# Performance work log

Hardware: AMD Instinct MI355X
Metric: run time of the kernel (lower is better)

The kernel has to match this reference:

```python
import jax, jax.numpy as jnp
import numpy as np

NEG_SLOPE = 0.2

def _gatv2_layer(x, src, tgt, Wl, Wr, att, bias, num_nodes, heads, ch):
    # x: [N, Fin]; src/tgt: [E] (self loops already included)
    xl = (x @ Wl).reshape(num_nodes, heads, ch)  # source transform [N,H,C]
    xr = (x @ Wr).reshape(num_nodes, heads, ch)  # target transform [N,H,C]
    m = xl[src] + xr[tgt]                        # [E,H,C]
    m = jnp.where(m > 0, m, NEG_SLOPE * m)       # LeakyReLU
    e = jnp.einsum('ehc,hc->eh', m, att)         # attention logits [E,H]
    # softmax over incoming edges of each target node (numerically stable)
    e_max = jax.ops.segment_max(e, tgt, num_segments=num_nodes)
    e_max = jnp.where(jnp.isfinite(e_max), e_max, 0.0)
    alpha = jnp.exp(e - e_max[tgt])              # [E,H]
    denom = jax.ops.segment_sum(alpha, tgt, num_segments=num_nodes)
    alpha = alpha / (denom[tgt] + 1e-16)
    out = jax.ops.segment_sum(alpha[:, :, None] * xl[src], tgt, num_segments=num_nodes)  # [N,H,C]
    return out.mean(axis=1) + bias               # concat=False -> mean over heads, then bias


def setup_inputs() -> dict:
    key = jax.random.key(0)
    ks = jax.random.split(key, 12)
    N, E = 50000, 800000
    IN, HID, H = 128, 64, 2
    features = jax.random.normal(ks[0], (N, IN), dtype=jnp.float32)
    edge_index = jax.random.randint(ks[1], (2, E), 0, N, dtype=jnp.int64)
    s = 0.1
    return {
        'features': features,
        'edge_index': edge_index,
        'Wl1': jax.random.normal(ks[2], (IN, H * HID), dtype=jnp.float32) * s,
        'Wr1': jax.random.normal(ks[3], (IN, H * HID), dtype=jnp.float32) * s,
        'att1': jax.random.normal(ks[4], (H, HID), dtype=jnp.float32) * s,
        'b1': jnp.zeros((HID,), dtype=jnp.float32),
        'Wl2': jax.random.normal(ks[5], (HID, H * HID), dtype=jnp.float32) * s,
        'Wr2': jax.random.normal(ks[6], (HID, H * HID), dtype=jnp.float32) * s,
        'att2': jax.random.normal(ks[7], (H, HID), dtype=jnp.float32) * s,
        'b2': jnp.zeros((HID,), dtype=jnp.float32),
    }


def reference(features, edge_index, Wl1, Wr1, att1, b1, Wl2, Wr2, att2, b2):
    N = features.shape[0]
    H, HID = att1.shape
    # PyG GATv2Conv default add_self_loops=True
    loop = jnp.arange(N, dtype=edge_index.dtype)
    src = jnp.concatenate([edge_index[0], loop])
    tgt = jnp.concatenate([edge_index[1], loop])
    h = _gatv2_layer(features, src, tgt, Wl1, Wr1, att1, b1, N, H, HID)
    h = jax.nn.relu(h)
    out = _gatv2_layer(h, src, tgt, Wl2, Wr2, att2, b2, N, H, HID)
    return out  # node_mask in original is None
```

## Files before the change

kernel.cpp:

```cpp
#include <hip/hip_runtime.h>
#include <hip/hip_bf16.h>
#include <math.h>


#define HEADS 2
#define CH 64
#define FDIM (HEADS * CH)
#define CAP 48
#define HBLK 3328

typedef _Float16 f16_t;
typedef _Float16 f16x4 __attribute__((ext_vector_type(4)));
typedef _Float16 f16x8 __attribute__((ext_vector_type(8)));
typedef float f32x4 __attribute__((ext_vector_type(4)));
typedef float f32x2 __attribute__((ext_vector_type(2)));


__global__ __launch_bounds__(256)
void init_kernel(const float* __restrict__ Wl1, const float* __restrict__ Wr1,
                 const float* __restrict__ Wl2, const float* __restrict__ Wr2,
                 f16_t* __restrict__ fl1, f16_t* __restrict__ fr1,
                 f16_t* __restrict__ fl2, f16_t* __restrict__ fr2,
                 int* __restrict__ cnt, int N) {
    int bx = blockIdx.x;
    if (bx < 4) {
        const float* W; f16_t* F; int K;
        switch (bx) {
            case 0:  W = Wl1; F = fl1; K = 128; break;
            case 1:  W = Wr1; F = fr1; K = 128; break;
            case 2:  W = Wl2; F = fl2; K = 64;  break;
            default: W = Wr2; F = fr2; K = 64;  break;
        }
        int S = K >> 5;
        int total = 8 * S * 64;
        for (int idx = threadIdx.x; idx < total; idx += blockDim.x) {
            int l  = idx & 63;
            int ts = idx >> 6;
            int s  = ts % S;
            int t  = ts / S;
            int n  = t * 16 + (l & 15);
            int k0 = s * 32 + (l >> 4) * 8;
            f16x8 v;
            #pragma unroll
            for (int j = 0; j < 8; ++j) v[j] = (f16_t)W[(size_t)(k0 + j) * 128 + n];
            *(f16x8*)(F + (size_t)idx * 8) = v;
        }
    } else {
        int n4 = (N + 3) >> 2;
        int stride = (gridDim.x - 4) * blockDim.x;
        for (int i = (bx - 4) * blockDim.x + threadIdx.x; i < n4; i += stride) {
            int i0 = i * 4;
            if (i0 + 3 < N) *(int4*)(cnt + i0) = make_int4(0, 0, 0, 0);
            else for (int k = 0; k < 4 && i0 + k < N; ++k) cnt[i0 + k] = 0;
        }
    }
}


__device__ __forceinline__ unsigned int pack_bf16x2(float x, float y) {
    __hip_bfloat16 lo = __float2bfloat16(x);
    __hip_bfloat16 hi = __float2bfloat16(y);
    unsigned short ulo = *reinterpret_cast<unsigned short*>(&lo);
    unsigned short uhi = *reinterpret_cast<unsigned short*>(&hi);
    return ((unsigned int)uhi << 16) | ulo;
}

__device__ __forceinline__
void gemm_body(const float* __restrict__ X,
               const f16_t* __restrict__ FL, const f16_t* __restrict__ FR,
               unsigned int* __restrict__ Y0b, float* __restrict__ Y1,
               int N, int K, int gblk, float* lds_f) {
    f16_t* Af = (f16_t*)lds_f;
    int tid  = threadIdx.x;
    int lane = tid & 63;
    int wave = tid >> 6;
    int row0 = gblk * 32;
    int S = K >> 5;

    {
        int r  = tid >> 3;
        int m  = r & 15;
        int g  = r >> 4;
        int gr = row0 + r;
        int kc = (tid & 7) * (K >> 3);
        const float* xp = X + (size_t)gr * K + kc;
        f16_t* areg = Af + g * (16 * K);
        for (int c = 0; c < (K >> 3); c += 4) {
            float4 xv = make_float4(0.f, 0.f, 0.f, 0.f);
            if (gr < N) xv = *(const float4*)(xp + c);
            int k = kc + c;
            int s = k >> 5;
            int lanei = ((k >> 3) & 3) * 16 + m;
            int j = k & 7;
            f16x4 h;
            h[0] = (f16_t)xv.x; h[1] = (f16_t)xv.y;
            h[2] = (f16_t)xv.z; h[3] = (f16_t)xv.w;
            *(f16x4*)(areg + ((s * 64 + lanei) * 8 + j)) = h;
        }
    }
    __syncthreads();

    int rg  = wave >> 1;
    int mat = wave & 1;
    const f16_t* F = mat ? FR : FL;

    f32x4 acc[8];
    #pragma unroll
    for (int t = 0; t < 8; ++t) acc[t] = (f32x4){0.f, 0.f, 0.f, 0.f};

    const f16_t* aw = Af + rg * (16 * K);
    for (int s = 0; s < S; ++s) {
        f16x8 a = *(const f16x8*)(aw + (s * 64 + lane) * 8);
        #pragma unroll
        for (int t = 0; t < 8; ++t) {
            f16x8 b = *(const f16x8*)(F + ((size_t)(t * S + s) * 64 + lane) * 8);
            acc[t] = __builtin_amdgcn_mfma_f32_16x16x32_f16(a, b, acc[t], 0, 0, 0);
        }
    }
    __syncthreads();

    float* ew = lds_f + wave * (16 * 68);
    int mrow = (lane >> 4) * 4;
    int ccol = lane & 15;
    int rr = lane & 15;
    int ch = lane >> 4;
    int gr2 = row0 + rg * 16 + rr;

    #pragma unroll
    for (int h = 0; h < 2; ++h) {
        #pragma unroll
        for (int tt = 0; tt < 4; ++tt)
            #pragma unroll
            for (int r = 0; r < 4; ++r)
                ew[(mrow + r) * 68 + tt * 16 + ccol] = acc[h * 4 + tt][r];
        __syncthreads();
        if (gr2 < N) {
            const float* src = ew + rr * 68 + ch * 16;
            if (mat == 0) {
                uint4 o0, o1;
                o0.x = pack_bf16x2(src[0],  src[1]);
                o0.y = pack_bf16x2(src[2],  src[3]);
                o0.z = pack_bf16x2(src[4],  src[5]);
                o0.w = pack_bf16x2(src[6],  src[7]);
                o1.x = pack_bf16x2(src[8],  src[9]);
                o1.y = pack_bf16x2(src[10], src[11]);
                o1.z = pack_bf16x2(src[12], src[13]);
                o1.w = pack_bf16x2(src[14], src[15]);
                unsigned int* dst = Y0b + (size_t)gr2 * (FDIM / 2) + h * 32 + ch * 8;
                *(uint4*)dst       = o0;
                *(uint4*)(dst + 4) = o1;
            } else {
                float* dst = Y1 + (size_t)gr2 * FDIM + h * 64 + ch * 16;
                #pragma unroll
                for (int q = 0; q < 4; ++q)
                    *(float4*)(dst + q * 4) = *(const float4*)(src + q * 4);
            }
        }
        __syncthreads();
    }
}

__global__ __launch_bounds__(256)
void fused_scatter_gemm_kernel(const float* __restrict__ X,
                               const f16_t* __restrict__ FL,
                               const f16_t* __restrict__ FR,
                               unsigned int* __restrict__ Y0b,
                               float* __restrict__ Y1,
                               int N, int K,
                               const int* __restrict__ ei, int* __restrict__ cnt,
                               int* __restrict__ ssrc, int E) {
    __shared__ float lds_f[4352];

    if (blockIdx.x < HBLK) {
        int vb   = blockIdx.x;
        int part = vb & 7;
        int blk  = vb >> 3;
        int nblk = HBLK >> 3;
        int lo = (int)(((long long)N * part) >> 3);
        int hi = (int)(((long long)N * (part + 1)) >> 3);
        int stride = nblk * blockDim.x;
        int G = E >> 2;
        for (int g = blk * blockDim.x + threadIdx.x; g < G; g += stride) {
            int4 t4 = *(const int4*)(ei + E + g * 4);
            if (t4.x >= lo && t4.x < hi) {
                int k = atomicAdd(&cnt[t4.x], 1);
                if (k < CAP) ssrc[t4.x * CAP + k] = ei[g * 4 + 0];
            }
            if (t4.y >= lo && t4.y < hi) {
                int k = atomicAdd(&cnt[t4.y], 1);
                if (k < CAP) ssrc[t4.y * CAP + k] = ei[g * 4 + 1];
            }
            if (t4.z >= lo && t4.z < hi) {
                int k = atomicAdd(&cnt[t4.z], 1);
                if (k < CAP) ssrc[t4.z * CAP + k] = ei[g * 4 + 2];
            }
            if (t4.w >= lo && t4.w < hi) {
                int k = atomicAdd(&cnt[t4.w], 1);
                if (k < CAP) ssrc[t4.w * CAP + k] = ei[g * 4 + 3];
            }
        }
        for (int e = (G << 2) + blk * blockDim.x + threadIdx.x; e < E; e += stride) {
            int t = ei[E + e];
            if (t >= lo && t < hi) {
                int k = atomicAdd(&cnt[t], 1);
                if (k < CAP) ssrc[t * CAP + k] = ei[e];
            }
        }
        for (int n = lo + blk * blockDim.x + threadIdx.x; n < hi; n += stride) {
            int k = atomicAdd(&cnt[n], 1);
            if (k < CAP) ssrc[n * CAP + k] = n;
        }
        return;
    }

    gemm_body(X, FL, FR, Y0b, Y1, N, K, blockIdx.x - HBLK, lds_f);
}

__global__ __launch_bounds__(256)
void gemm_kernel(const float* __restrict__ X,
                 const f16_t* __restrict__ FL, const f16_t* __restrict__ FR,
                 unsigned int* __restrict__ Y0b, float* __restrict__ Y1,
                 int N, int K) {
    __shared__ float lds_f[4352];
    gemm_body(X, FL, FR, Y0b, Y1, N, K, blockIdx.x, lds_f);
}


__device__ __forceinline__ f32x2 unpk2(unsigned int u) {
    f32x2 r;
    r.x = __uint_as_float(u << 16);
    r.y = __uint_as_float(u & 0xFFFF0000u);
    return r;
}

__device__ __forceinline__ f32x2 lrelu2v(f32x2 t) {
    f32x2 m = t * 0.2f;
    t.x = fmaxf(t.x, m.x);
    t.y = fmaxf(t.y, m.y);
    return t;
}

__device__ __forceinline__
float2 agg_node(const unsigned int* __restrict__ xlb, const float* __restrict__ xr,
                const int* __restrict__ cnt, const int* __restrict__ ssrc,
                f32x2 a2, int node, int lane) {
    f32x2 xr2 = *(const f32x2*)(xr + (size_t)node * FDIM + 2 * lane);

    int beg = node * CAP;
    int deg = cnt[node];
    deg = min(deg, CAP);

    float l = 0.f;
    f32x2 acc = (f32x2){0.f, 0.f};

    bool b0 = (lane & 1) != 0;
    bool b1 = (lane & 2) != 0;
    bool b2 = (lane & 4) != 0;
    int base = lane & 32;

    int nfull = deg & ~7;

    unsigned int u0, u1, u2, u3, u4, u5, u6, u7;
    if (nfull > 0) {
        int4 sA = *(const int4*)(ssrc + beg);
        int4 sB = *(const int4*)(ssrc + beg + 4);
        u0 = xlb[(size_t)sA.x * (FDIM / 2) + lane];
        u1 = xlb[(size_t)sA.y * (FDIM / 2) + lane];
        u2 = xlb[(size_t)sA.z * (FDIM / 2) + lane];
        u3 = xlb[(size_t)sA.w * (FDIM / 2) + lane];
        u4 = xlb[(size_t)sB.x * (FDIM / 2) + lane];
        u5 = xlb[(size_t)sB.y * (FDIM / 2) + lane];
        u6 = xlb[(size_t)sB.z * (FDIM / 2) + lane];
        u7 = xlb[(size_t)sB.w * (FDIM / 2) + lane];
    }
    for (int i = 0; i < nfull; i += 8) {
        unsigned int n0, n1, n2, n3, n4r, n5, n6, n7;
        bool more = (i + 8) < nfull;
        if (more) {
            int4 sA = *(const int4*)(ssrc + beg + i + 8);
            int4 sB = *(const int4*)(ssrc + beg + i + 12);
            n0 = xlb[(size_t)sA.x * (FDIM / 2) + lane];
            n1 = xlb[(size_t)sA.y * (FDIM / 2) + lane];
            n2 = xlb[(size_t)sA.z * (FDIM / 2) + lane];
            n3 = xlb[(size_t)sA.w * (FDIM / 2) + lane];
            n4r = xlb[(size_t)sB.x * (FDIM / 2) + lane];
            n5 = xlb[(size_t)sB.y * (FDIM / 2) + lane];
            n6 = xlb[(size_t)sB.z * (FDIM / 2) + lane];
            n7 = xlb[(size_t)sB.w * (FDIM / 2) + lane];
        }

        f32x2 v0 = unpk2(u0), v1 = unpk2(u1), v2 = unpk2(u2), v3 = unpk2(u3);
        f32x2 v4 = unpk2(u4), v5 = unpk2(u5), v6 = unpk2(u6), v7 = unpk2(u7);

        f32x2 t0 = lrelu2v(v0 + xr2);
        f32x2 t1 = lrelu2v(v1 + xr2);
        f32x2 t2 = lrelu2v(v2 + xr2);
        f32x2 t3 = lrelu2v(v3 + xr2);
        f32x2 t4 = lrelu2v(v4 + xr2);
        f32x2 t5 = lrelu2v(v5 + xr2);
        f32x2 t6 = lrelu2v(v6 + xr2);
        f32x2 t7 = lrelu2v(v7 + xr2);
        float p0 = fmaf(t0.x, a2.x, t0.y * a2.y);
        float p1 = fmaf(t1.x, a2.x, t1.y * a2.y);
        float p2 = fmaf(t2.x, a2.x, t2.y * a2.y);
        float p3 = fmaf(t3.x, a2.x, t3.y * a2.y);
        float p4 = fmaf(t4.x, a2.x, t4.y * a2.y);
        float p5 = fmaf(t5.x, a2.x, t5.y * a2.y);
        float p6 = fmaf(t6.x, a2.x, t6.y * a2.y);
        float p7 = fmaf(t7.x, a2.x, t7.y * a2.y);

        float s01 = (b0 ? p1 : p0) + __shfl_xor(b0 ? p0 : p1, 1, 64);
        float s23 = (b0 ? p3 : p2) + __shfl_xor(b0 ? p2 : p3, 1, 64);
        float s45 = (b0 ? p5 : p4) + __shfl_xor(b0 ? p4 : p5, 1, 64);
        float s67 = (b0 ? p7 : p6) + __shfl_xor(b0 ? p6 : p7, 1, 64);
        float q03 = (b1 ? s23 : s01) + __shfl_xor(b1 ? s01 : s23, 2, 64);
        float q47 = (b1 ? s67 : s45) + __shfl_xor(b1 ? s45 : s67, 2, 64);
        float r = (b2 ? q47 : q03) + __shfl_xor(b2 ? q03 : q47, 4, 64);
        r += __shfl_xor(r, 8, 64);
        r += __shfl_xor(r, 16, 64);

        float a = __expf(r);
        float al0 = __shfl(a, base | 0, 64);
        float al1 = __shfl(a, base | 1, 64);
        float al2 = __shfl(a, base | 2, 64);
        float al3 = __shfl(a, base | 3, 64);
        float al4 = __shfl(a, base | 4, 64);
        float al5 = __shfl(a, base | 5, 64);
        float al6 = __shfl(a, base | 6, 64);
        float al7 = __shfl(a, base | 7, 64);

        acc = v0 * al0 + acc;
        acc = v1 * al1 + acc;
        acc = v2 * al2 + acc;
        acc = v3 * al3 + acc;
        acc = v4 * al4 + acc;
        acc = v5 * al5 + acc;
        acc = v6 * al6 + acc;
        acc = v7 * al7 + acc;
        l += ((al0 + al1) + (al2 + al3)) + ((al4 + al5) + (al6 + al7));

        if (more) {
            u0 = n0; u1 = n1; u2 = n2; u3 = n3;
            u4 = n4r; u5 = n5; u6 = n6; u7 = n7;
        }
    }

    int i = beg + nfull;
    int end = beg + deg;
    int n4c = i + ((end - i) & ~3);
    for (; i < n4c; i += 4) {
        int4 sA = *(const int4*)(ssrc + i);
        unsigned int w0 = xlb[(size_t)sA.x * (FDIM / 2) + lane];
        unsigned int w1 = xlb[(size_t)sA.y * (FDIM / 2) + lane];
        unsigned int w2 = xlb[(size_t)sA.z * (FDIM / 2) + lane];
        unsigned int w3 = xlb[(size_t)sA.w * (FDIM / 2) + lane];
        f32x2 v0 = unpk2(w0), v1 = unpk2(w1), v2 = unpk2(w2), v3 = unpk2(w3);

        f32x2 t0 = lrelu2v(v0 + xr2);
        f32x2 t1 = lrelu2v(v1 + xr2);
        f32x2 t2 = lrelu2v(v2 + xr2);
        f32x2 t3 = lrelu2v(v3 + xr2);
        float p0 = fmaf(t0.x, a2.x, t0.y * a2.y);
        float p1 = fmaf(t1.x, a2.x, t1.y * a2.y);
        float p2 = fmaf(t2.x, a2.x, t2.y * a2.y);
        float p3 = fmaf(t3.x, a2.x, t3.y * a2.y);

        float s01 = (b0 ? p1 : p0) + __shfl_xor(b0 ? p0 : p1, 1, 64);
        float s23 = (b0 ? p3 : p2) + __shfl_xor(b0 ? p2 : p3, 1, 64);
        float q = (b1 ? s23 : s01) + __shfl_xor(b1 ? s01 : s23, 2, 64);
        q += __shfl_xor(q, 4, 64);
        q += __shfl_xor(q, 8, 64);
        q += __shfl_xor(q, 16, 64);
        float a = __expf(q);
        float al0 = __shfl(a, base | 0, 64);
        float al1 = __shfl(a, base | 1, 64);
        float al2 = __shfl(a, base | 2, 64);
        float al3 = __shfl(a, base | 3, 64);

        acc = v0 * al0 + acc;
        acc = v1 * al1 + acc;
        acc = v2 * al2 + acc;
        acc = v3 * al3 + acc;
        l += (al0 + al1) + (al2 + al3);
    }
    for (; i < end; ++i) {
        int s = ssrc[i];
        unsigned int u = xlb[(size_t)s * (FDIM / 2) + lane];
        f32x2 v = unpk2(u);
        f32x2 t = lrelu2v(v + xr2);
        float p = fmaf(t.x, a2.x, t.y * a2.y);
        #pragma unroll
        for (int d = 1; d < 32; d <<= 1) p += __shfl_xor(p, d, 64);
        float al = __expf(p);
        acc = v * al + acc;
        l += al;
    }

    float inv = 1.0f / (l + 1e-16f);
    return make_float2(acc.x * inv, acc.y * inv);
}

__global__ __launch_bounds__(256)
void agg_kernel(const unsigned int* __restrict__ xlb, const float* __restrict__ xr,
                const int* __restrict__ cnt, const int* __restrict__ ssrc,
                const float* __restrict__ att, const float* __restrict__ bias,
                float* __restrict__ out, int N, int do_relu) {
    int node = blockIdx.x * 4 + (threadIdx.x >> 6);
    int lane = threadIdx.x & 63;
    if (node >= N) return;

    f32x2 a2 = *(const f32x2*)(att + 2 * lane);
    float2 r = agg_node(xlb, xr, cnt, ssrc, a2, node, lane);
    float ox = 0.5f * (r.x + __shfl_xor(r.x, 32, 64));
    float oy = 0.5f * (r.y + __shfl_xor(r.y, 32, 64));
    if (lane < 32) {
        float2 b = *(const float2*)(bias + 2 * lane);
        ox += b.x; oy += b.y;
        if (do_relu) { ox = fmaxf(ox, 0.f); oy = fmaxf(oy, 0.f); }
        *(float2*)(out + (size_t)node * CH + 2 * lane) = make_float2(ox, oy);
    }
}


__global__ __launch_bounds__(256)
void agg_gemm4_kernel(const unsigned int* __restrict__ xlb, const float* __restrict__ xr,
                      const int* __restrict__ cnt, const int* __restrict__ ssrc,
                      const float* __restrict__ att, const float* __restrict__ bias,
                      const f16_t* __restrict__ FL, const f16_t* __restrict__ FR,
                      unsigned int* __restrict__ Y0b, float* __restrict__ Y1, int N) {
    __shared__ float hrows[4 * 68];
    __shared__ f16_t Af[16 * 64];

    int tid  = threadIdx.x;
    int lane = tid & 63;
    int wave = tid >> 6;
    int row0 = blockIdx.x * 4;
    int node = row0 + wave;

    f32x2 a2 = *(const f32x2*)(att + 2 * lane);
    float2 bv = make_float2(0.f, 0.f);
    if (lane < 32) bv = *(const float2*)(bias + 2 * lane);

    float ox = 0.f, oy = 0.f;
    if (node < N) {
        float2 r = agg_node(xlb, xr, cnt, ssrc, a2, node, lane);
        ox = 0.5f * (r.x + __shfl_xor(r.x, 32, 64));
        oy = 0.5f * (r.y + __shfl_xor(r.y, 32, 64));
        ox = fmaxf(ox + bv.x, 0.f);
        oy = fmaxf(oy + bv.y, 0.f);
    }
    if (lane < 32)
        *(float2*)(hrows + wave * 68 + 2 * lane) = make_float2(ox, oy);
    __syncthreads();

    if (tid < 32) {
        int r  = tid >> 3;
        int kc = (tid & 7) * 8;
        const float* xp = hrows + r * 68 + kc;
        #pragma unroll
        for (int c = 0; c < 8; c += 4) {
            float4 xv = *(const float4*)(xp + c);
            int k = kc + c;
            int s = k >> 5;
            int lanei = ((k >> 3) & 3) * 16 + r;
            int j = k & 7;
            f16x4 h;
            h[0] = (f16_t)xv.x; h[1] = (f16_t)xv.y;
            h[2] = (f16_t)xv.z; h[3] = (f16_t)xv.w;
            *(f16x4*)(Af + ((s * 64 + lanei) * 8 + j)) = h;
        }
    }
    __syncthreads();

    const f16_t* F = (wave < 2) ? FL : FR;
    int tbase = (wave & 1) * 4;
    f32x4 acc[4];
    #pragma unroll
    for (int t = 0; t < 4; ++t) acc[t] = (f32x4){0.f, 0.f, 0.f, 0.f};
    #pragma unroll
    for (int s = 0; s < 2; ++s) {
        f16x8 a = *(const f16x8*)(Af + (s * 64 + lane) * 8);
        #pragma unroll
        for (int tt = 0; tt < 4; ++tt) {
            f16x8 b = *(const f16x8*)(F + ((size_t)((tbase + tt) * 2 + s) * 64 + lane) * 8);
            acc[tt] = __builtin_amdgcn_mfma_f32_16x16x32_f16(a, b, acc[tt], 0, 0, 0);
        }
    }

    int mrow = (lane >> 4) * 4;
    int ccol = lane & 15;
    #pragma unroll
    for (int tt = 0; tt < 4; ++tt) {
        int t = tbase + tt;
        #pragma unroll
        for (int r = 0; r < 4; ++r) {
            float v = acc[tt][r];
            float wv = __shfl_xor(v, 1, 64);
            int grow = row0 + mrow + r;
            if (mrow == 0 && grow < N) {
                if (wave < 2) {
                    if (!(lane & 1))
                        Y0b[(size_t)grow * (FDIM / 2) + t * 8 + (ccol >> 1)] = pack_bf16x2(v, wv);
                } else {
                    Y1[(size_t)grow * FDIM + t * 16 + ccol] = v;
                }
            }
        }
    }
}


static inline size_t align_up(size_t x, size_t a) { return (x + a - 1) & ~(a - 1); }

extern "C" void kernel_launch(void* const* d_in, const int* in_sizes, int n_in,
                              void* d_out, int out_size, void* d_ws, size_t ws_size,
                              hipStream_t stream) {
    const float* features = (const float*)d_in[0];
    const int*   ei       = (const int*)d_in[1];
    const float* Wl1      = (const float*)d_in[2];
    const float* Wr1      = (const float*)d_in[3];
    const float* att1     = (const float*)d_in[4];
    const float* b1       = (const float*)d_in[5];
    const float* Wl2      = (const float*)d_in[6];
    const float* Wr2      = (const float*)d_in[7];
    const float* att2     = (const float*)d_in[8];
    const float* b2       = (const float*)d_in[9];

    int N = in_sizes[0] / FDIM;
    int E = in_sizes[1] / 2;

    size_t sz_cnt  = align_up((size_t)N * 4, 256);
    size_t sz_ssrc = align_up((size_t)N * CAP * 4, 256);
    size_t sz_xlb  = align_up((size_t)N * (FDIM / 2) * 4, 256);
    size_t sz_xr   = align_up((size_t)N * FDIM * 4, 256);
    size_t sz_h    = align_up((size_t)N * CH * 4, 256);
    size_t sz_f128 = align_up((size_t)8 * 4 * 64 * 8 * 2, 256);
    size_t sz_f64  = align_up((size_t)8 * 2 * 64 * 8 * 2, 256);

    char* w = (char*)d_ws;
    int* cnt          = (int*)w;          w += sz_cnt;
    int* ssrc         = (int*)w;          w += sz_ssrc;
    unsigned int* xlb = (unsigned int*)w; w += sz_xlb;
    float* xr         = (float*)w;        w += sz_xr;

    size_t need_fused = sz_cnt + sz_ssrc + 2 * sz_xlb + 2 * sz_xr
                      + 2 * sz_f128 + 2 * sz_f64;

    int gblocks = (N + 31) / 32;
    dim3 agrid((N + 3) / 4);

    if (ws_size >= need_fused) {
        unsigned int* xlb2 = (unsigned int*)w; w += sz_xlb;
        float* xr2         = (float*)w;        w += sz_xr;
        f16_t* fl1 = (f16_t*)w; w += sz_f128;
        f16_t* fr1 = (f16_t*)w; w += sz_f128;
        f16_t* fl2 = (f16_t*)w; w += sz_f64;
        f16_t* fr2 = (f16_t*)w; w += sz_f64;

        init_kernel<<<56, 256, 0, stream>>>(Wl1, Wr1, Wl2, Wr2,
                                            fl1, fr1, fl2, fr2, cnt, N);
        fused_scatter_gemm_kernel<<<HBLK + gblocks, 256, 0, stream>>>(
            features, fl1, fr1, xlb, xr, N, 128, ei, cnt, ssrc, E);
        agg_gemm4_kernel<<<agrid, 256, 0, stream>>>(
            xlb, xr, cnt, ssrc, att1, b1, fl2, fr2, xlb2, xr2, N);
        agg_kernel<<<agrid, 256, 0, stream>>>(
            xlb2, xr2, cnt, ssrc, att2, b2, (float*)d_out, N, 0);
    } else {
        float* hbuf = (float*)w; w += sz_h;
        f16_t* fl1 = (f16_t*)w; w += sz_f128;
        f16_t* fr1 = (f16_t*)w; w += sz_f128;
        f16_t* fl2 = (f16_t*)w; w += sz_f64;
        f16_t* fr2 = (f16_t*)w; w += sz_f64;

        init_kernel<<<56, 256, 0, stream>>>(Wl1, Wr1, Wl2, Wr2,
                                            fl1, fr1, fl2, fr2, cnt, N);
        fused_scatter_gemm_kernel<<<HBLK + gblocks, 256, 0, stream>>>(
            features, fl1, fr1, xlb, xr, N, 128, ei, cnt, ssrc, E);
        agg_kernel<<<agrid, 256, 0, stream>>>(xlb, xr, cnt, ssrc, att1, b1, hbuf, N, 1);
        gemm_kernel<<<gblocks, 256, 0, stream>>>(hbuf, fl2, fr2, xlb, xr, N, 64);
        agg_kernel<<<agrid, 256, 0, stream>>>(xlb, xr, cnt, ssrc, att2, b2, (float*)d_out, N, 0);
    }
}
```

Before: 282.8 us.

## Prefetch edge indices two chunks ahead and drop fused agg-gemm path

The aggregation loop now loads source indices two chunks ahead, so the gather addresses for the next chunk are ready without a dependent index load. A sched_barrier is added to keep the prefetch loads ahead of the compute. The fused layer-1 aggregation plus GEMM kernel and its workspace branch are removed, so the program always runs separate agg, gemm and agg kernels with an hbuf round trip. The separate path adds a kernel launch and extra global traffic but gives each kernel its full occupancy.

After: 279.7 us. About the same (-1.1%).

```diff
diff --git a/kernel.cpp b/kernel.cpp
--- a/kernel.cpp
+++ b/kernel.cpp
@@ -258,36 +258,45 @@
     bool b2 = (lane & 4) != 0;
     int base = lane & 32;
 
-    int nfull = deg & ~7;
+    int nchunk = deg >> 3;
 
     unsigned int u0, u1, u2, u3, u4, u5, u6, u7;
-    if (nfull > 0) {
-        int4 sA = *(const int4*)(ssrc + beg);
-        int4 sB = *(const int4*)(ssrc + beg + 4);
-        u0 = xlb[(size_t)sA.x * (FDIM / 2) + lane];
-        u1 = xlb[(size_t)sA.y * (FDIM / 2) + lane];
-        u2 = xlb[(size_t)sA.z * (FDIM / 2) + lane];
-        u3 = xlb[(size_t)sA.w * (FDIM / 2) + lane];
-        u4 = xlb[(size_t)sB.x * (FDIM / 2) + lane];
-        u5 = xlb[(size_t)sB.y * (FDIM / 2) + lane];
-        u6 = xlb[(size_t)sB.z * (FDIM / 2) + lane];
-        u7 = xlb[(size_t)sB.w * (FDIM / 2) + lane];
-    }
-    for (int i = 0; i < nfull; i += 8) {
+    int4 iA, iB;
+    if (nchunk > 0) {
+        int4 cA = *(const int4*)(ssrc + beg);
+        int4 cB = *(const int4*)(ssrc + beg + 4);
+        u0 = xlb[(size_t)cA.x * (FDIM / 2) + lane];
+        u1 = xlb[(size_t)cA.y * (FDIM / 2) + lane];
+        u2 = xlb[(size_t)cA.z * (FDIM / 2) + lane];
+        u3 = xlb[(size_t)cA.w * (FDIM / 2) + lane];
+        u4 = xlb[(size_t)cB.x * (FDIM / 2) + lane];
+        u5 = xlb[(size_t)cB.y * (FDIM / 2) + lane];
+        u6 = xlb[(size_t)cB.z * (FDIM / 2) + lane];
+        u7 = xlb[(size_t)cB.w * (FDIM / 2) + lane];
+        if (nchunk > 1) {
+            iA = *(const int4*)(ssrc + beg + 8);
+            iB = *(const int4*)(ssrc + beg + 12);
+        }
+    }
+
+    for (int c = 0; c < nchunk; ++c) {
         unsigned int n0, n1, n2, n3, n4r, n5, n6, n7;
-        bool more = (i + 8) < nfull;
+        bool more = (c + 1) < nchunk;
         if (more) {
-            int4 sA = *(const int4*)(ssrc + beg + i + 8);
-            int4 sB = *(const int4*)(ssrc + beg + i + 12);
-            n0 = xlb[(size_t)sA.x * (FDIM / 2) + lane];
-            n1 = xlb[(size_t)sA.y * (FDIM / 2) + lane];
-            n2 = xlb[(size_t)sA.z * (FDIM / 2) + lane];
-            n3 = xlb[(size_t)sA.w * (FDIM / 2) + lane];
-            n4r = xlb[(size_t)sB.x * (FDIM / 2) + lane];
-            n5 = xlb[(size_t)sB.y * (FDIM / 2) + lane];
-            n6 = xlb[(size_t)sB.z * (FDIM / 2) + lane];
-            n7 = xlb[(size_t)sB.w * (FDIM / 2) + lane];
-        }
+            n0 = xlb[(size_t)iA.x * (FDIM / 2) + lane];
+            n1 = xlb[(size_t)iA.y * (FDIM / 2) + lane];
+            n2 = xlb[(size_t)iA.z * (FDIM / 2) + lane];
+            n3 = xlb[(size_t)iA.w * (FDIM / 2) + lane];
+            n4r = xlb[(size_t)iB.x * (FDIM / 2) + lane];
+            n5 = xlb[(size_t)iB.y * (FDIM / 2) + lane];
+            n6 = xlb[(size_t)iB.z * (FDIM / 2) + lane];
+            n7 = xlb[(size_t)iB.w * (FDIM / 2) + lane];
+            if (c + 2 < nchunk) {
+                iA = *(const int4*)(ssrc + beg + (c + 2) * 8);
+                iB = *(const int4*)(ssrc + beg + (c + 2) * 8 + 4);
+            }
+        }
+        __builtin_amdgcn_sched_barrier(0);
 
         f32x2 v0 = unpk2(u0), v1 = unpk2(u1), v2 = unpk2(u2), v3 = unpk2(u3);
         f32x2 v4 = unpk2(u4), v5 = unpk2(u5), v6 = unpk2(u6), v7 = unpk2(u7);
@@ -345,7 +354,7 @@
         }
     }
 
-    int i = beg + nfull;
+    int i = beg + (nchunk << 3);
     int end = beg + deg;
     int n4c = i + ((end - i) & ~3);
     for (; i < n4c; i += 4) {
@@ -418,94 +427,6 @@
         ox += b.x; oy += b.y;
         if (do_relu) { ox = fmaxf(ox, 0.f); oy = fmaxf(oy, 0.f); }
         *(float2*)(out + (size_t)node * CH + 2 * lane) = make_float2(ox, oy);
-    }
-}
-
-
-__global__ __launch_bounds__(256)
-void agg_gemm4_kernel(const unsigned int* __restrict__ xlb, const float* __restrict__ xr,
-                      const int* __restrict__ cnt, const int* __restrict__ ssrc,
-                      const float* __restrict__ att, const float* __restrict__ bias,
-                      const f16_t* __restrict__ FL, const f16_t* __restrict__ FR,
-                      unsigned int* __restrict__ Y0b, float* __restrict__ Y1, int N) {
-    __shared__ float hrows[4 * 68];
-    __shared__ f16_t Af[16 * 64];
-
-    int tid  = threadIdx.x;
-    int lane = tid & 63;
-    int wave = tid >> 6;
-    int row0 = blockIdx.x * 4;
-    int node = row0 + wave;
-
-    f32x2 a2 = *(const f32x2*)(att + 2 * lane);
-    float2 bv = make_float2(0.f, 0.f);
-    if (lane < 32) bv = *(const float2*)(bias + 2 * lane);
-
-    float ox = 0.f, oy = 0.f;
-    if (node < N) {
-        float2 r = agg_node(xlb, xr, cnt, ssrc, a2, node, lane);
-        ox = 0.5f * (r.x + __shfl_xor(r.x, 32, 64));
-        oy = 0.5f * (r.y + __shfl_xor(r.y, 32, 64));
-        ox = fmaxf(ox + bv.x, 0.f);
-        oy = fmaxf(oy + bv.y, 0.f);
-    }
-    if (lane < 32)
-        *(float2*)(hrows + wave * 68 + 2 * lane) = make_float2(ox, oy);
-    __syncthreads();
-
-    if (tid < 32) {
-        int r  = tid >> 3;
-        int kc = (tid & 7) * 8;
-        const float* xp = hrows + r * 68 + kc;
-        #pragma unroll
-        for (int c = 0; c < 8; c += 4) {
-            float4 xv = *(const float4*)(xp + c);
-            int k = kc + c;
-            int s = k >> 5;
-            int lanei = ((k >> 3) & 3) * 16 + r;
-            int j = k & 7;
-            f16x4 h;
-            h[0] = (f16_t)xv.x; h[1] = (f16_t)xv.y;
-            h[2] = (f16_t)xv.z; h[3] = (f16_t)xv.w;
-            *(f16x4*)(Af + ((s * 64 + lanei) * 8 + j)) = h;
-        }
-    }
-    __syncthreads();
-
-    const f16_t* F = (wave < 2) ? FL : FR;
-    int tbase = (wave & 1) * 4;
-    f32x4 acc[4];
-    #pragma unroll
-    for (int t = 0; t < 4; ++t) acc[t] = (f32x4){0.f, 0.f, 0.f, 0.f};
-    #pragma unroll
-    for (int s = 0; s < 2; ++s) {
-        f16x8 a = *(const f16x8*)(Af + (s * 64 + lane) * 8);
-        #pragma unroll
-        for (int tt = 0; tt < 4; ++tt) {
-            f16x8 b = *(const f16x8*)(F + ((size_t)((tbase + tt) * 2 + s) * 64 + lane) * 8);
-            acc[tt] = __builtin_amdgcn_mfma_f32_16x16x32_f16(a, b, acc[tt], 0, 0, 0);
-        }
-    }
-
-    int mrow = (lane >> 4) * 4;
-    int ccol = lane & 15;
-    #pragma unroll
-    for (int tt = 0; tt < 4; ++tt) {
-        int t = tbase + tt;
-        #pragma unroll
-        for (int r = 0; r < 4; ++r) {
-            float v = acc[tt][r];
-            float wv = __shfl_xor(v, 1, 64);
-            int grow = row0 + mrow + r;
-            if (mrow == 0 && grow < N) {
-                if (wave < 2) {
-                    if (!(lane & 1))
-                        Y0b[(size_t)grow * (FDIM / 2) + t * 8 + (ccol >> 1)] = pack_bf16x2(v, wv);
-                } else {
-                    Y1[(size_t)grow * FDIM + t * 16 + ccol] = v;
-                }
-            }
-        }
     }
 }
 
@@ -529,55 +450,27 @@
     int N = in_sizes[0] / FDIM;
     int E = in_sizes[1] / 2;
 
-    size_t sz_cnt  = align_up((size_t)N * 4, 256);
-    size_t sz_ssrc = align_up((size_t)N * CAP * 4, 256);
-    size_t sz_xlb  = align_up((size_t)N * (FDIM / 2) * 4, 256);
-    size_t sz_xr   = align_up((size_t)N * FDIM * 4, 256);
-    size_t sz_h    = align_up((size_t)N * CH * 4, 256);
-    size_t sz_f128 = align_up((size_t)8 * 4 * 64 * 8 * 2, 256);
-    size_t sz_f64  = align_up((size_t)8 * 2 * 64 * 8 * 2, 256);
-
     char* w = (char*)d_ws;
-    int* cnt          = (int*)w;          w += sz_cnt;
-    int* ssrc         = (int*)w;          w += sz_ssrc;
-    unsigned int* xlb = (unsigned int*)w; w += sz_xlb;
-    float* xr         = (float*)w;        w += sz_xr;
-
-    size_t need_fused = sz_cnt + sz_ssrc + 2 * sz_xlb + 2 * sz_xr
-                      + 2 * sz_f128 + 2 * sz_f64;
+    int* cnt      = (int*)w;  w += align_up((size_t)N * 4, 256);
+    int* ssrc     = (int*)w;  w += align_up((size_t)N * CAP * 4, 256);
+    unsigned int* xlb = (unsigned int*)w; w += align_up((size_t)N * (FDIM / 2) * 4, 256);
+    float* xr     = (float*)w; w += align_up((size_t)N * FDIM * 4, 256);
+    float* hbuf   = (float*)w; w += align_up((size_t)N * CH * 4, 256);
+    f16_t* fl1    = (f16_t*)w; w += align_up((size_t)8 * 4 * 64 * 8 * 2, 256);
+    f16_t* fr1    = (f16_t*)w; w += align_up((size_t)8 * 4 * 64 * 8 * 2, 256);
+    f16_t* fl2    = (f16_t*)w; w += align_up((size_t)8 * 2 * 64 * 8 * 2, 256);
+    f16_t* fr2    = (f16_t*)w; w += align_up((size_t)8 * 2 * 64 * 8 * 2, 256);
 
     int gblocks = (N + 31) / 32;
     dim3 agrid((N + 3) / 4);
 
-    if (ws_size >= need_fused) {
-        unsigned int* xlb2 = (unsigned int*)w; w += sz_xlb;
-        float* xr2         = (float*)w;        w += sz_xr;
-        f16_t* fl1 = (f16_t*)w; w += sz_f128;
-        f16_t* fr1 = (f16_t*)w; w += sz_f128;
-        f16_t* fl2 = (f16_t*)w; w += sz_f64;
-        f16_t* fr2 = (f16_t*)w; w += sz_f64;
-
-        init_kernel<<<56, 256, 0, stream>>>(Wl1, Wr1, Wl2, Wr2,
-                                            fl1, fr1, fl2, fr2, cnt, N);
-        fused_scatter_gemm_kernel<<<HBLK + gblocks, 256, 0, stream>>>(
-            features, fl1, fr1, xlb, xr, N, 128, ei, cnt, ssrc, E);
-        agg_gemm4_kernel<<<agrid, 256, 0, stream>>>(
-            xlb, xr, cnt, ssrc, att1, b1, fl2, fr2, xlb2, xr2, N);
-        agg_kernel<<<agrid, 256, 0, stream>>>(
-            xlb2, xr2, cnt, ssrc, att2, b2, (float*)d_out, N, 0);
-    } else {
-        float* hbuf = (float*)w; w += sz_h;
-        f16_t* fl1 = (f16_t*)w; w += sz_f128;
-        f16_t* fr1 = (f16_t*)w; w += sz_f128;
-        f16_t* fl2 = (f16_t*)w; w += sz_f64;
-        f16_t* fr2 = (f16_t*)w; w += sz_f64;
-
-        init_kernel<<<56, 256, 0, stream>>>(Wl1, Wr1, Wl2, Wr2,
-                                            fl1, fr1, fl2, fr2, cnt, N);
-        fused_scatter_gemm_kernel<<<HBLK + gblocks, 256, 0, stream>>>(
-            features, fl1, fr1, xlb, xr, N, 128, ei, cnt, ssrc, E);
-        agg_kernel<<<agrid, 256, 0, stream>>>(xlb, xr, cnt, ssrc, att1, b1, hbuf, N, 1);
-        gemm_kernel<<<gblocks, 256, 0, stream>>>(hbuf, fl2, fr2, xlb, xr, N, 64);
-        agg_kernel<<<agrid, 256, 0, stream>>>(xlb, xr, cnt, ssrc, att2, b2, (float*)d_out, N, 0);
-    }
-}
+    init_kernel<<<56, 256, 0, stream>>>(Wl1, Wr1, Wl2, Wr2,
+                                        fl1, fr1, fl2, fr2, cnt, N);
+
+    fused_scatter_gemm_kernel<<<HBLK + gblocks, 256, 0, stream>>>(
+        features, fl1, fr1, xlb, xr, N, 128, ei, cnt, ssrc, E);
+    agg_kernel<<<agrid, 256, 0, stream>>>(xlb, xr, cnt, ssrc, att1, b1, hbuf, N, 1);
+
+    gemm_kernel<<<gblocks, 256, 0, stream>>>(hbuf, fl2, fr2, xlb, xr, N, 64);
+    agg_kernel<<<agrid, 256, 0, stream>>>(xlb, xr, cnt, ssrc, att2, b2, (float*)d_out, N, 0);
+}
```
